# Performance work log

Measured on AMD Instinct MI355X. Metric: run time of the kernel, lower is better.

## Reference

```python
import jax, jax.numpy as jnp
import numpy as np

B, N_IN, K_OUT, C_IN, C_OUT = 32, 2048, 128, 16, 16
NUM_ITERS = 3


def squash_v1(x, axis):
    s2 = (x ** 2).sum(axis, keepdims=True)
    return (jnp.sqrt(s2) / (0.5 + s2)) * x


def setup_inputs() -> dict:
    key = jax.random.key(0)
    k1, k2, k3 = jax.random.split(key, 3)
    x = jax.random.normal(k1, (B, N_IN, C_IN), dtype=jnp.float32)
    y = jax.random.normal(k2, (B, K_OUT), dtype=jnp.float32)  # unused by forward
    labels = jnp.arange(K_OUT, dtype=jnp.int64)
    # xavier-uniform-ish init for W1 [N_in, K_out, out_ch, in_ch] (leading 1 dropped)
    bound = float(np.sqrt(6.0 / (C_IN + C_OUT)))
    W1 = jax.random.uniform(k3, (N_IN, K_OUT, C_OUT, C_IN), dtype=jnp.float32,
                            minval=-bound, maxval=bound)
    return {"x": x, "y": y, "labels": labels, "W1": W1}


def reference(x, y, labels, W1):
    # select output capsules, then u_hat[b,i,k,d] = sum_c W[i,k,d,c] * x[b,i,c]
    W = W1[:, labels]                                   # [N, K, D, C]
    u_hat = jnp.einsum('ikdc,bic->bikd', W, x)          # [B, N, K, D]
    u_sq = squash_v1(u_hat, axis=-1)                    # reused each iteration
    b = jnp.zeros(u_hat.shape[:3], dtype=u_hat.dtype)   # [B, N, K]
    v = None
    for i in range(NUM_ITERS):
        c = jax.nn.softmax(b, axis=2)                   # over output capsules
        c = c / c.sum(axis=1, keepdims=True)            # normalize over input caps
        v = squash_v1(jnp.einsum('bik,bikd->bkd', c, u_hat), axis=-1)  # [B, K, D]
        if i < NUM_ITERS - 1:
            dd = 1.0 - ((u_sq - v[:, None]) ** 2).sum(-1)  # [B, N, K]
            b = b + dd
    poses = v                                           # [B, K, D]
    activations = jnp.sqrt((poses ** 2).sum(-1))        # [B, K]
    return poses, activations
```

## Files before the change

kernel.cpp:

```cpp
#include <hip/hip_runtime.h>


typedef __attribute__((ext_vector_type(8))) short  s16x8;
typedef __attribute__((ext_vector_type(4))) float  f32x4;

#define NSLICE 64

__device__ __forceinline__ unsigned bf16rn(float f) {
    const unsigned u = __builtin_bit_cast(unsigned, f);
    return (u + 0x7fffu + ((u >> 16) & 1u)) >> 16;
}
__device__ __forceinline__ unsigned pack2rn(float a, float b) {
    return bf16rn(a) | (bf16rn(b) << 16);
}
__device__ __forceinline__ unsigned phi(float a, float b) {
    return (__builtin_bit_cast(unsigned, a) >> 16) | (__builtin_bit_cast(unsigned, b) & 0xffff0000u);
}
__device__ __forceinline__ unsigned plo(float a, float b) {
    const float la = a - __builtin_bit_cast(float, __builtin_bit_cast(unsigned, a) & 0xffff0000u);
    const float lb = b - __builtin_bit_cast(float, __builtin_bit_cast(unsigned, b) & 0xffff0000u);
    return pack2rn(la, lb);
}

__device__ __forceinline__ void pack_A(const float* __restrict__ xp, s16x8& A1, s16x8& A2) {
    const float4 x0 = *(const float4*)xp;
    const float4 x1 = *(const float4*)(xp + 4);
    uint4 h, l;
    h.x = phi(x0.x, x0.y); h.y = phi(x0.z, x0.w);
    h.z = phi(x1.x, x1.y); h.w = phi(x1.z, x1.w);
    l.x = plo(x0.x, x0.y); l.y = plo(x0.z, x0.w);
    l.z = plo(x1.x, x1.y); l.w = plo(x1.z, x1.w);
    A1 = __builtin_bit_cast(s16x8, h);
    A2 = __builtin_bit_cast(s16x8, l);
}

__device__ __forceinline__ s16x8 pack_B(const float* __restrict__ wp, bool sel) {
    const float4 w0 = *(const float4*)wp;
    const float4 w1 = *(const float4*)(wp + 4);
    const float f[8] = {w0.x, w0.y, w0.z, w0.w, w1.x, w1.y, w1.z, w1.w};
    float t[8];
#pragma unroll
    for (int j = 0; j < 8; ++j) {
        const float hf = __builtin_bit_cast(float, __builtin_bit_cast(unsigned, f[j]) & 0xffff0000u);
        t[j] = sel ? hf : (f[j] - hf);
    }
    uint4 bw;
    bw.x = pack2rn(t[0], t[1]);
    bw.y = pack2rn(t[2], t[3]);
    bw.z = pack2rn(t[4], t[5]);
    bw.w = pack2rn(t[6], t[7]);
    return __builtin_bit_cast(s16x8, bw);
}

__global__ __launch_bounds__(256) void k_packW(const float* __restrict__ W,
                                               s16x8* __restrict__ Wp)
{
    const size_t gid = (size_t)blockIdx.x * 256 + threadIdx.x;
    const size_t ik  = gid >> 6;
    const int lane = threadIdx.x & 63;
    const int n    = lane & 15, q = lane >> 4;
    const int oct  = (q & 1) * 8;
    const bool sel = (q < 2);
    Wp[ik * 64 + lane] = pack_B(W + ik * 256 + n * 16 + oct, sel);
}

__global__ __launch_bounds__(256) void k_packX(const float* __restrict__ x,
                                               s16x8* __restrict__ xA)
{
    const int wid  = blockIdx.x * 4 + (threadIdx.x >> 6);
    const int lane = threadIdx.x & 63;
    const int i  = wid >> 1, bg = wid & 1;
    const int n  = lane & 15, q = lane >> 4;
    const int oct = (q & 1) * 8;
    s16x8 A1, A2;
    pack_A(x + ((size_t)(bg * 16 + n) * 2048 + i) * 16 + oct, A1, A2);
    s16x8* o = xA + ((size_t)wid * 64 + lane) * 2;
    o[0] = A1;
    o[1] = A2;
}

template<bool USE_P, bool PK>
__global__ __launch_bounds__(256) void k_acc(const float* __restrict__ W,
                                             const float* __restrict__ x,
                                             const s16x8* __restrict__ Wp,
                                             const s16x8* __restrict__ xA,
                                             const float* __restrict__ p,
                                             float* __restrict__ out_sl,
                                             float* __restrict__ csl)
{
    const int w    = blockIdx.x * 4 + (threadIdx.x >> 6);
    const int lane = threadIdx.x & 63;
    const int n    = lane & 15;
    const int q    = lane >> 4;
    const int oct  = (q & 1) * 8;
    const bool sel = (q < 2);
    const int k0    = (w & 63) * 2;
    const int slice = w >> 6;
    const int i0    = slice * 32;

    const f32x4 zero = {0.f, 0.f, 0.f, 0.f};
    f32x4 acc[2][2];
    float csacc[2][2];
#pragma unroll
    for (int kp = 0; kp < 2; ++kp)
#pragma unroll
        for (int bg = 0; bg < 2; ++bg) { acc[kp][bg] = zero; csacc[kp][bg] = 0.f; }

#pragma unroll 1
    for (int i = i0; i < i0 + 32; ++i) {
        s16x8 X1[2], X2[2];
        if constexpr (PK) {
            const s16x8* xp = xA + ((size_t)i * 2 * 64 + lane) * 2;
            X1[0] = xp[0];   X2[0] = xp[1];
            X1[1] = xp[128]; X2[1] = xp[129];
        } else {
#pragma unroll
            for (int bg = 0; bg < 2; ++bg)
                pack_A(x + ((size_t)(bg * 16 + n) * 2048 + i) * 16 + oct, X1[bg], X2[bg]);
        }
#pragma unroll
        for (int kp = 0; kp < 2; ++kp) {
            const int k = k0 + kp;
            const s16x8 Wf = PK ? Wp[((size_t)i * 128 + k) * 64 + lane]
                                : pack_B(W + (size_t)i * 32768 + (size_t)k * 256 + n * 16 + oct, sel);
#pragma unroll
            for (int bg = 0; bg < 2; ++bg) {
                if (USE_P) {
                    f32x4 u = __builtin_amdgcn_mfma_f32_16x16x32_bf16(Wf, X1[bg], zero, 0, 0, 0);
                    u       = __builtin_amdgcn_mfma_f32_16x16x32_bf16(Wf, X2[bg], u,    0, 0, 0);
                    const float pv = p[((size_t)i * 128 + k) * 32 + bg * 16 + n];
                    acc[kp][bg].x = fmaf(pv, u.x, acc[kp][bg].x);
                    acc[kp][bg].y = fmaf(pv, u.y, acc[kp][bg].y);
                    acc[kp][bg].z = fmaf(pv, u.z, acc[kp][bg].z);
                    acc[kp][bg].w = fmaf(pv, u.w, acc[kp][bg].w);
                    csacc[kp][bg] += pv;
                } else {
                    acc[kp][bg] = __builtin_amdgcn_mfma_f32_16x16x32_bf16(Wf, X1[bg], acc[kp][bg], 0, 0, 0);
                    acc[kp][bg] = __builtin_amdgcn_mfma_f32_16x16x32_bf16(Wf, X2[bg], acc[kp][bg], 0, 0, 0);
                }
            }
        }
    }
#pragma unroll
    for (int kp = 0; kp < 2; ++kp)
#pragma unroll
        for (int bg = 0; bg < 2; ++bg)
            *(f32x4*)(out_sl + (((size_t)slice * 32 + bg * 16 + n) * 128 + (k0 + kp)) * 16 + 4 * q)
                = acc[kp][bg];
    if (USE_P && lane < 16) {
#pragma unroll
        for (int kp = 0; kp < 2; ++kp)
#pragma unroll
            for (int bg = 0; bg < 2; ++bg)
                csl[((size_t)slice * 128 + (k0 + kp)) * 32 + bg * 16 + n] = csacc[kp][bg];
    }
}

template<bool PK>
__global__ __launch_bounds__(512) void k_logits(const float* __restrict__ W,
                                                const float* __restrict__ x,
                                                const s16x8* __restrict__ Wp,
                                                const s16x8* __restrict__ xA,
                                                const float* __restrict__ Vq,
                                                const float* __restrict__ Nt,
                                                const float T,
                                                float* __restrict__ pbuf)
{
    __shared__ __align__(16) float e_s[8][16][32];
    __shared__ __align__(16) float den_s[8][32];
    __shared__ float denom_s[32];
    const int tid  = threadIdx.x;
    const int wv   = tid >> 6, lane = tid & 63;
    const int n    = lane & 15, q = lane >> 4;
    const int oct  = (q & 1) * 8;
    const bool sel = (q < 2);
    const f32x4 zero = {0.f, 0.f, 0.f, 0.f};

    const int pk = tid >> 2;
    const int pb = (tid & 3) * 8;

    const int i0 = blockIdx.x * 4;
#pragma unroll 1
    for (int ii = 0; ii < 4; ++ii) {
        const int i = i0 + ii;
        s16x8 X1[2], X2[2];
        if constexpr (PK) {
            const s16x8* xp = xA + ((size_t)i * 2 * 64 + lane) * 2;
            X1[0] = xp[0];   X2[0] = xp[1];
            X1[1] = xp[128]; X2[1] = xp[129];
        } else {
#pragma unroll
            for (int bg = 0; bg < 2; ++bg)
                pack_A(x + ((size_t)(bg * 16 + n) * 2048 + i) * 16 + oct, X1[bg], X2[bg]);
        }

        float den0 = 0.f, den1 = 0.f;
#pragma unroll
        for (int kp = 0; kp < 16; ++kp) {
            const int k = wv * 16 + kp;
            const s16x8 Wf = PK ? Wp[((size_t)i * 128 + k) * 64 + lane]
                                : pack_B(W + (size_t)i * 32768 + (size_t)k * 256 + n * 16 + oct, sel);
            float ebg[2];
#pragma unroll
            for (int bg = 0; bg < 2; ++bg) {
                f32x4 u = __builtin_amdgcn_mfma_f32_16x16x32_bf16(Wf, X1[bg], zero, 0, 0, 0);
                u       = __builtin_amdgcn_mfma_f32_16x16x32_bf16(Wf, X2[bg], u,    0, 0, 0);
                const float4 Vv = *(const float4*)(Vq + (((size_t)k * 4 + q) * 32 + bg * 16 + n) * 4);
                float s2 = u.x * u.x;
                s2 = fmaf(u.y, u.y, s2);
                s2 = fmaf(u.z, u.z, s2);
                s2 = fmaf(u.w, u.w, s2);
                float dt = u.x * Vv.x;
                dt = fmaf(u.y, Vv.y, dt);
                dt = fmaf(u.z, Vv.z, dt);
                dt = fmaf(u.w, Vv.w, dt);
                s2 += __shfl_xor(s2, 16, 64);
                s2 += __shfl_xor(s2, 32, 64);
                dt += __shfl_xor(dt, 16, 64);
                dt += __shfl_xor(dt, 32, 64);
                const float Nr  = Nt[(size_t)k * 32 + bg * 16 + n];
                const float inv = 1.0f / (0.5f + s2);
                const float scl = sqrtf(s2) * inv;
                const float fq  = s2 * s2 * inv * inv;
                const float e   = __expf(T * (1.0f - fq) + 2.0f * scl * dt - Nr);
                if (bg == 0) den0 += e; else den1 += e;
                ebg[bg] = e;
            }
            if (lane < 16) {
                e_s[wv][kp][n]      = ebg[0];
                e_s[wv][kp][16 + n] = ebg[1];
            }
        }
        if (lane < 16) {
            den_s[wv][n]      = den0;
            den_s[wv][16 + n] = den1;
        }
        __syncthreads();
        if (tid < 32) {
            float s = 0.f;
#pragma unroll
            for (int w2 = 0; w2 < 8; ++w2) s += den_s[w2][tid];
            denom_s[tid] = s;
        }
        __syncthreads();
        {
            const float4 e0 = *(const float4*)&e_s[pk >> 4][pk & 15][pb];
            const float4 e1 = *(const float4*)&e_s[pk >> 4][pk & 15][pb + 4];
            const float4 d0 = *(const float4*)&denom_s[pb];
            const float4 d1 = *(const float4*)&denom_s[pb + 4];
            float4 p0, p1;
            p0.x = e0.x / d0.x; p0.y = e0.y / d0.y; p0.z = e0.z / d0.z; p0.w = e0.w / d0.w;
            p1.x = e1.x / d1.x; p1.y = e1.y / d1.y; p1.z = e1.z / d1.z; p1.w = e1.w / d1.w;
            *(float4*)(pbuf + ((size_t)i * 128 + pk) * 32 + pb)     = p0;
            *(float4*)(pbuf + ((size_t)i * 128 + pk) * 32 + pb + 4) = p1;
        }
        __syncthreads();
    }
}

__global__ __launch_bounds__(256) void k_fin(const float* __restrict__ raw_sl,
                                             const float* __restrict__ csl,
                                             const float* __restrict__ Vq_prev,
                                             const float* __restrict__ Nt_prev,
                                             float* __restrict__ Vq_out,
                                             float* __restrict__ Nt_out,
                                             float* __restrict__ out,
                                             const int mode)
{
    const int tid = threadIdx.x;
    const int t   = blockIdx.x * 16 + (tid >> 4);
    const int d   = tid & 15;
    const int b   = t >> 7, k = t & 127;
    float s = 0.f, cs = 0.f;
    if (mode == 0) {
#pragma unroll 4
        for (int sl = 0; sl < NSLICE; ++sl) s += raw_sl[(size_t)sl * 65536 + (size_t)t * 16 + d];
    } else {
#pragma unroll 4
        for (int sl = 0; sl < NSLICE; ++sl) {
            s  += raw_sl[(size_t)sl * 65536 + (size_t)t * 16 + d];
            cs += csl[(size_t)sl * 4096 + k * 32 + b];
        }
    }
    const float invcs = (mode == 0) ? (1.0f / 2048.0f) : 1.0f / cs;
    const float v = s * invcs;
    float s2 = v * v;
#pragma unroll
    for (int m = 1; m < 16; m <<= 1) s2 += __shfl_xor(s2, m, 64);
    const float inv = 1.0f / (0.5f + s2);
    const float scl = sqrtf(s2) * inv;
    const size_t vidx = (((size_t)k * 4 + (d >> 2)) * 32 + b) * 4 + (d & 3);
    if (mode == 0) {
        Vq_out[vidx] = scl * v;
        if (d == 0) Nt_out[(size_t)k * 32 + b] = s2 * scl * scl;
    } else if (mode == 1) {
        Vq_out[vidx] = Vq_prev[vidx] + scl * v;
        if (d == 0) Nt_out[(size_t)k * 32 + b] = Nt_prev[(size_t)k * 32 + b] + s2 * scl * scl;
    } else {
        out[(size_t)t * 16 + d] = scl * v;
        if (d == 0) out[65536 + t] = s2 * inv;
    }
}

extern "C" void kernel_launch(void* const* d_in, const int* in_sizes, int n_in,
                              void* d_out, int out_size, void* d_ws, size_t ws_size,
                              hipStream_t stream)
{
    const float* x = (const float*)d_in[0];
    const float* W = (const float*)d_in[3];

    float* ws    = (float*)d_ws;
    float* Vbt0  = ws;
    float* VSbt  = ws + 65536;
    float* N1t   = ws + 131072;
    float* N2t   = ws + 135168;
    float* csl   = ws + 139264;
    float* pbuf  = ws + 401408;
    float* slces = ws + 8790016;

    s16x8* Wp = (s16x8*)(ws + 12984320);
    s16x8* xA = (s16x8*)((short*)Wp + (size_t)134217728);
    const size_t needed = (size_t)12984320 * 4
                        + (size_t)134217728 * 2
                        + (size_t)8388608 * 2;
    const bool pk = (ws_size >= needed);

    if (pk) {
        k_packW<<<65536, 256, 0, stream>>>(W, Wp);
        k_packX<<<1024, 256, 0, stream>>>(x, xA);
        k_acc<false, true><<<1024, 256, 0, stream>>>(W, x, Wp, xA, nullptr, slces, nullptr);
        k_fin<<<256, 256, 0, stream>>>(slces, nullptr, nullptr, nullptr, Vbt0, N1t, nullptr, 0);
        k_logits<true><<<512, 512, 0, stream>>>(W, x, Wp, xA, Vbt0, N1t, 1.0f, pbuf);
        k_acc<true, true><<<1024, 256, 0, stream>>>(W, x, Wp, xA, pbuf, slces, csl);
        k_fin<<<256, 256, 0, stream>>>(slces, csl, Vbt0, N1t, VSbt, N2t, nullptr, 1);
        k_logits<true><<<512, 512, 0, stream>>>(W, x, Wp, xA, VSbt, N2t, 2.0f, pbuf);
        k_acc<true, true><<<1024, 256, 0, stream>>>(W, x, Wp, xA, pbuf, slces, csl);
        k_fin<<<256, 256, 0, stream>>>(slces, csl, nullptr, nullptr, nullptr, nullptr, (float*)d_out, 2);
    } else {
        k_acc<false, false><<<1024, 256, 0, stream>>>(W, x, nullptr, nullptr, nullptr, slces, nullptr);
        k_fin<<<256, 256, 0, stream>>>(slces, nullptr, nullptr, nullptr, Vbt0, N1t, nullptr, 0);
        k_logits<false><<<512, 512, 0, stream>>>(W, x, nullptr, nullptr, Vbt0, N1t, 1.0f, pbuf);
        k_acc<true, false><<<1024, 256, 0, stream>>>(W, x, nullptr, nullptr, pbuf, slces, csl);
        k_fin<<<256, 256, 0, stream>>>(slces, csl, Vbt0, N1t, VSbt, N2t, nullptr, 1);
        k_logits<false><<<512, 512, 0, stream>>>(W, x, nullptr, nullptr, VSbt, N2t, 2.0f, pbuf);
        k_acc<true, false><<<1024, 256, 0, stream>>>(W, x, nullptr, nullptr, pbuf, slces, csl);
        k_fin<<<256, 256, 0, stream>>>(slces, csl, nullptr, nullptr, nullptr, nullptr, (float*)d_out, 2);
    }
}
```

Baseline: 858.4 us.

## Fuse W packing into first accumulation pass and software-pipeline loads

```diff
diff --git a/kernel.cpp b/kernel.cpp
--- a/kernel.cpp
+++ b/kernel.cpp
@@ -34,9 +34,7 @@
     A2 = __builtin_bit_cast(s16x8, l);
 }
 
-__device__ __forceinline__ s16x8 pack_B(const float* __restrict__ wp, bool sel) {
-    const float4 w0 = *(const float4*)wp;
-    const float4 w1 = *(const float4*)(wp + 4);
+__device__ __forceinline__ s16x8 pack_B_f(const float4 w0, const float4 w1, bool sel) {
     const float f[8] = {w0.x, w0.y, w0.z, w0.w, w1.x, w1.y, w1.z, w1.w};
     float t[8];
 #pragma unroll
@@ -51,17 +49,8 @@
     bw.w = pack2rn(t[6], t[7]);
     return __builtin_bit_cast(s16x8, bw);
 }
-
-__global__ __launch_bounds__(256) void k_packW(const float* __restrict__ W,
-                                               s16x8* __restrict__ Wp)
-{
-    const size_t gid = (size_t)blockIdx.x * 256 + threadIdx.x;
-    const size_t ik  = gid >> 6;
-    const int lane = threadIdx.x & 63;
-    const int n    = lane & 15, q = lane >> 4;
-    const int oct  = (q & 1) * 8;
-    const bool sel = (q < 2);
-    Wp[ik * 64 + lane] = pack_B(W + ik * 256 + n * 16 + oct, sel);
+__device__ __forceinline__ s16x8 pack_B(const float* __restrict__ wp, bool sel) {
+    return pack_B_f(*(const float4*)wp, *(const float4*)(wp + 4), sel);
 }
 
 __global__ __launch_bounds__(256) void k_packX(const float* __restrict__ x,
@@ -79,14 +68,10 @@
     o[1] = A2;
 }
 
-template<bool USE_P, bool PK>
-__global__ __launch_bounds__(256) void k_acc(const float* __restrict__ W,
-                                             const float* __restrict__ x,
-                                             const s16x8* __restrict__ Wp,
-                                             const s16x8* __restrict__ xA,
-                                             const float* __restrict__ p,
-                                             float* __restrict__ out_sl,
-                                             float* __restrict__ csl)
+__global__ __launch_bounds__(256) void k_packWacc(const float* __restrict__ W,
+                                                  const s16x8* __restrict__ xA,
+                                                  s16x8* __restrict__ Wp,
+                                                  float* __restrict__ out_sl)
 {
     const int w    = blockIdx.x * 4 + (threadIdx.x >> 6);
     const int lane = threadIdx.x & 63;
@@ -100,43 +85,177 @@
 
     const f32x4 zero = {0.f, 0.f, 0.f, 0.f};
     f32x4 acc[2][2];
-    float csacc[2][2];
 #pragma unroll
     for (int kp = 0; kp < 2; ++kp)
 #pragma unroll
-        for (int bg = 0; bg < 2; ++bg) { acc[kp][bg] = zero; csacc[kp][bg] = 0.f; }
+        for (int bg = 0; bg < 2; ++bg) acc[kp][bg] = zero;
+
+    float4 rw0[2], rw1[2];
+    s16x8 X1c[2], X2c[2];
+    {
+        const float* wp_ = W + (size_t)i0 * 32768 + (size_t)k0 * 256 + n * 16 + oct;
+        rw0[0] = *(const float4*)wp_;          rw1[0] = *(const float4*)(wp_ + 4);
+        rw0[1] = *(const float4*)(wp_ + 256);  rw1[1] = *(const float4*)(wp_ + 260);
+        const s16x8* xp = xA + (size_t)i0 * 256 + (size_t)lane * 2;
+        X1c[0] = xp[0];   X2c[0] = xp[1];
+        X1c[1] = xp[128]; X2c[1] = xp[129];
+    }
 
 #pragma unroll 1
     for (int i = i0; i < i0 + 32; ++i) {
-        s16x8 X1[2], X2[2];
-        if constexpr (PK) {
-            const s16x8* xp = xA + ((size_t)i * 2 * 64 + lane) * 2;
-            X1[0] = xp[0];   X2[0] = xp[1];
-            X1[1] = xp[128]; X2[1] = xp[129];
-        } else {
+        const int in_ = (i + 1 < i0 + 32) ? i + 1 : i;
+        float4 nw0[2], nw1[2];
+        s16x8 X1n[2], X2n[2];
+        {
+            const float* wp_ = W + (size_t)in_ * 32768 + (size_t)k0 * 256 + n * 16 + oct;
+            nw0[0] = *(const float4*)wp_;          nw1[0] = *(const float4*)(wp_ + 4);
+            nw0[1] = *(const float4*)(wp_ + 256);  nw1[1] = *(const float4*)(wp_ + 260);
+            const s16x8* xp = xA + (size_t)in_ * 256 + (size_t)lane * 2;
+            X1n[0] = xp[0];   X2n[0] = xp[1];
+            X1n[1] = xp[128]; X2n[1] = xp[129];
+        }
+#pragma unroll
+        for (int kp = 0; kp < 2; ++kp) {
+            const s16x8 Wf = pack_B_f(rw0[kp], rw1[kp], sel);
+            Wp[((size_t)i * 128 + (k0 + kp)) * 64 + lane] = Wf;
+#pragma unroll
+            for (int bg = 0; bg < 2; ++bg) {
+                acc[kp][bg] = __builtin_amdgcn_mfma_f32_16x16x32_bf16(Wf, X1c[bg], acc[kp][bg], 0, 0, 0);
+                acc[kp][bg] = __builtin_amdgcn_mfma_f32_16x16x32_bf16(Wf, X2c[bg], acc[kp][bg], 0, 0, 0);
+            }
+        }
+#pragma unroll
+        for (int kp = 0; kp < 2; ++kp) { rw0[kp] = nw0[kp]; rw1[kp] = nw1[kp]; }
+#pragma unroll
+        for (int bg = 0; bg < 2; ++bg) { X1c[bg] = X1n[bg]; X2c[bg] = X2n[bg]; }
+    }
+#pragma unroll
+    for (int kp = 0; kp < 2; ++kp)
+#pragma unroll
+        for (int bg = 0; bg < 2; ++bg)
+            *(f32x4*)(out_sl + (((size_t)slice * 32 + bg * 16 + n) * 128 + (k0 + kp)) * 16 + 4 * q)
+                = acc[kp][bg];
+}
+
+template<bool USE_P, bool PK>
+__global__ __launch_bounds__(256) void k_acc(const float* __restrict__ W,
+                                             const float* __restrict__ x,
+                                             const s16x8* __restrict__ Wp,
+                                             const s16x8* __restrict__ xA,
+                                             const float* __restrict__ p,
+                                             float* __restrict__ out_sl,
+                                             float* __restrict__ csl)
+{
+    const int w    = blockIdx.x * 4 + (threadIdx.x >> 6);
+    const int lane = threadIdx.x & 63;
+    const int n    = lane & 15;
+    const int q    = lane >> 4;
+    const int oct  = (q & 1) * 8;
+    const bool sel = (q < 2);
+    const int k0    = (w & 63) * 2;
+    const int slice = w >> 6;
+    const int i0    = slice * 32;
+
+    const f32x4 zero = {0.f, 0.f, 0.f, 0.f};
+    f32x4 acc[2][2];
+    float csacc[2][2];
+#pragma unroll
+    for (int kp = 0; kp < 2; ++kp)
+#pragma unroll
+        for (int bg = 0; bg < 2; ++bg) { acc[kp][bg] = zero; csacc[kp][bg] = 0.f; }
+
+    if constexpr (PK) {
+        s16x8 X1c[2], X2c[2], Wc[2];
+        float pc[2][2];
+        {
+            const s16x8* xp = xA + (size_t)i0 * 256 + (size_t)lane * 2;
+            X1c[0] = xp[0];   X2c[0] = xp[1];
+            X1c[1] = xp[128]; X2c[1] = xp[129];
+            Wc[0] = Wp[((size_t)i0 * 128 + k0) * 64 + lane];
+            Wc[1] = Wp[((size_t)i0 * 128 + k0 + 1) * 64 + lane];
+            if (USE_P) {
+#pragma unroll
+                for (int kp = 0; kp < 2; ++kp)
+#pragma unroll
+                    for (int bg = 0; bg < 2; ++bg)
+                        pc[kp][bg] = p[((size_t)i0 * 128 + k0 + kp) * 32 + bg * 16 + n];
+            }
+        }
+#pragma unroll 1
+        for (int i = i0; i < i0 + 32; ++i) {
+            const int in_ = (i + 1 < i0 + 32) ? i + 1 : i;
+            s16x8 X1n[2], X2n[2], Wn[2];
+            float pn[2][2];
+            {
+                const s16x8* xp = xA + (size_t)in_ * 256 + (size_t)lane * 2;
+                X1n[0] = xp[0];   X2n[0] = xp[1];
+                X1n[1] = xp[128]; X2n[1] = xp[129];
+                Wn[0] = Wp[((size_t)in_ * 128 + k0) * 64 + lane];
+                Wn[1] = Wp[((size_t)in_ * 128 + k0 + 1) * 64 + lane];
+                if (USE_P) {
+#pragma unroll
+                    for (int kp = 0; kp < 2; ++kp)
+#pragma unroll
+                        for (int bg = 0; bg < 2; ++bg)
+                            pn[kp][bg] = p[((size_t)in_ * 128 + k0 + kp) * 32 + bg * 16 + n];
+                }
+            }
+#pragma unroll
+            for (int kp = 0; kp < 2; ++kp) {
+#pragma unroll
+                for (int bg = 0; bg < 2; ++bg) {
+                    if (USE_P) {
+                        f32x4 u = __builtin_amdgcn_mfma_f32_16x16x32_bf16(Wc[kp], X1c[bg], zero, 0, 0, 0);
+                        u       = __builtin_amdgcn_mfma_f32_16x16x32_bf16(Wc[kp], X2c[bg], u,    0, 0, 0);
+                        const float pv = pc[kp][bg];
+                        acc[kp][bg].x = fmaf(pv, u.x, acc[kp][bg].x);
+                        acc[kp][bg].y = fmaf(pv, u.y, acc[kp][bg].y);
+                        acc[kp][bg].z = fmaf(pv, u.z, acc[kp][bg].z);
+                        acc[kp][bg].w = fmaf(pv, u.w, acc[kp][bg].w);
+                        csacc[kp][bg] += pv;
+                    } else {
+                        acc[kp][bg] = __builtin_amdgcn_mfma_f32_16x16x32_bf16(Wc[kp], X1c[bg], acc[kp][bg], 0, 0, 0);
+                        acc[kp][bg] = __builtin_amdgcn_mfma_f32_16x16x32_bf16(Wc[kp], X2c[bg], acc[kp][bg], 0, 0, 0);
+                    }
+                }
+            }
+#pragma unroll
+            for (int kp = 0; kp < 2; ++kp) Wc[kp] = Wn[kp];
+#pragma unroll
+            for (int bg = 0; bg < 2; ++bg) { X1c[bg] = X1n[bg]; X2c[bg] = X2n[bg]; }
+            if (USE_P) {
+#pragma unroll
+                for (int kp = 0; kp < 2; ++kp)
+#pragma unroll
+                    for (int bg = 0; bg < 2; ++bg) pc[kp][bg] = pn[kp][bg];
+            }
+        }
+    } else {
+#pragma unroll 1
+        for (int i = i0; i < i0 + 32; ++i) {
+            s16x8 X1[2], X2[2];
 #pragma unroll
             for (int bg = 0; bg < 2; ++bg)
                 pack_A(x + ((size_t)(bg * 16 + n) * 2048 + i) * 16 + oct, X1[bg], X2[bg]);
-        }
-#pragma unroll
-        for (int kp = 0; kp < 2; ++kp) {
-            const int k = k0 + kp;
-            const s16x8 Wf = PK ? Wp[((size_t)i * 128 + k) * 64 + lane]
-                                : pack_B(W + (size_t)i * 32768 + (size_t)k * 256 + n * 16 + oct, sel);
-#pragma unroll
-            for (int bg = 0; bg < 2; ++bg) {
-                if (USE_P) {
-                    f32x4 u = __builtin_amdgcn_mfma_f32_16x16x32_bf16(Wf, X1[bg], zero, 0, 0, 0);
-                    u       = __builtin_amdgcn_mfma_f32_16x16x32_bf16(Wf, X2[bg], u,    0, 0, 0);
-                    const float pv = p[((size_t)i * 128 + k) * 32 + bg * 16 + n];
-                    acc[kp][bg].x = fmaf(pv, u.x, acc[kp][bg].x);
-                    acc[kp][bg].y = fmaf(pv, u.y, acc[kp][bg].y);
-                    acc[kp][bg].z = fmaf(pv, u.z, acc[kp][bg].z);
-                    acc[kp][bg].w = fmaf(pv, u.w, acc[kp][bg].w);
-                    csacc[kp][bg] += pv;
-                } else {
-                    acc[kp][bg] = __builtin_amdgcn_mfma_f32_16x16x32_bf16(Wf, X1[bg], acc[kp][bg], 0, 0, 0);
-                    acc[kp][bg] = __builtin_amdgcn_mfma_f32_16x16x32_bf16(Wf, X2[bg], acc[kp][bg], 0, 0, 0);
+#pragma unroll
+            for (int kp = 0; kp < 2; ++kp) {
+                const int k = k0 + kp;
+                const s16x8 Wf = pack_B(W + (size_t)i * 32768 + (size_t)k * 256 + n * 16 + oct, sel);
+#pragma unroll
+                for (int bg = 0; bg < 2; ++bg) {
+                    if (USE_P) {
+                        f32x4 u = __builtin_amdgcn_mfma_f32_16x16x32_bf16(Wf, X1[bg], zero, 0, 0, 0);
+                        u       = __builtin_amdgcn_mfma_f32_16x16x32_bf16(Wf, X2[bg], u,    0, 0, 0);
+                        const float pv = p[((size_t)i * 128 + k) * 32 + bg * 16 + n];
+                        acc[kp][bg].x = fmaf(pv, u.x, acc[kp][bg].x);
+                        acc[kp][bg].y = fmaf(pv, u.y, acc[kp][bg].y);
+                        acc[kp][bg].z = fmaf(pv, u.z, acc[kp][bg].z);
+                        acc[kp][bg].w = fmaf(pv, u.w, acc[kp][bg].w);
+                        csacc[kp][bg] += pv;
+                    } else {
+                        acc[kp][bg] = __builtin_amdgcn_mfma_f32_16x16x32_bf16(Wf, X1[bg], acc[kp][bg], 0, 0, 0);
+                        acc[kp][bg] = __builtin_amdgcn_mfma_f32_16x16x32_bf16(Wf, X2[bg], acc[kp][bg], 0, 0, 0);
+                    }
                 }
             }
         }
@@ -185,7 +304,7 @@
         const int i = i0 + ii;
         s16x8 X1[2], X2[2];
         if constexpr (PK) {
-            const s16x8* xp = xA + ((size_t)i * 2 * 64 + lane) * 2;
+            const s16x8* xp = xA + (size_t)i * 256 + (size_t)lane * 2;
             X1[0] = xp[0];   X2[0] = xp[1];
             X1[1] = xp[128]; X2[1] = xp[129];
         } else {
@@ -195,11 +314,19 @@
         }
 
         float den0 = 0.f, den1 = 0.f;
+        s16x8 Wf;
+        if constexpr (PK) Wf = Wp[((size_t)i * 128 + wv * 16) * 64 + lane];
 #pragma unroll
         for (int kp = 0; kp < 16; ++kp) {
             const int k = wv * 16 + kp;
-            const s16x8 Wf = PK ? Wp[((size_t)i * 128 + k) * 64 + lane]
-                                : pack_B(W + (size_t)i * 32768 + (size_t)k * 256 + n * 16 + oct, sel);
+            if constexpr (!PK) {
+                Wf = pack_B(W + (size_t)i * 32768 + (size_t)k * 256 + n * 16 + oct, sel);
+            }
+            s16x8 Wfn;
+            if constexpr (PK) {
+                const int kn = (kp < 15) ? k + 1 : k;
+                Wfn = Wp[((size_t)i * 128 + kn) * 64 + lane];
+            }
             float ebg[2];
 #pragma unroll
             for (int bg = 0; bg < 2; ++bg) {
@@ -230,6 +357,7 @@
                 e_s[wv][kp][n]      = ebg[0];
                 e_s[wv][kp][16 + n] = ebg[1];
             }
+            if constexpr (PK) Wf = Wfn;
         }
         if (lane < 16) {
             den_s[wv][n]      = den0;
@@ -326,9 +454,8 @@
     const bool pk = (ws_size >= needed);
 
     if (pk) {
-        k_packW<<<65536, 256, 0, stream>>>(W, Wp);
         k_packX<<<1024, 256, 0, stream>>>(x, xA);
-        k_acc<false, true><<<1024, 256, 0, stream>>>(W, x, Wp, xA, nullptr, slces, nullptr);
+        k_packWacc<<<1024, 256, 0, stream>>>(W, xA, Wp, slces);
         k_fin<<<256, 256, 0, stream>>>(slces, nullptr, nullptr, nullptr, Vbt0, N1t, nullptr, 0);
         k_logits<true><<<512, 512, 0, stream>>>(W, x, Wp, xA, Vbt0, N1t, 1.0f, pbuf);
         k_acc<true, true><<<1024, 256, 0, stream>>>(W, x, Wp, xA, pbuf, slces, csl);
```

New measurement: 780.9 us. 1.1x faster.
